# Kernel tuning notes

Hardware: AMD Instinct MI355X
Metric: run time of the kernel (lower is better)

The kernel has to match this reference:

```python
import jax, jax.numpy as jnp
import numpy as np

B, D_IN, UNITS = 4096, 1024, 1024


def setup_inputs() -> dict:
    key = jax.random.key(0)
    ks = jax.random.split(key, 8)
    scale = 1.0 / np.sqrt(D_IN + UNITS)
    return {
        "inputs": jax.random.normal(ks[0], (B, D_IN), jnp.float32),
        "hidden_state": jax.random.normal(ks[1], (B, UNITS), jnp.float32),
        "cell_state": jax.random.normal(ks[2], (B, UNITS), jnp.float32),
        "W_f": jax.random.normal(ks[3], (D_IN + UNITS, UNITS), jnp.float32) * scale,
        "b_f": jnp.ones((UNITS,), jnp.float32),  # forget gate bias initialized to ones
        "W_i": jax.random.normal(ks[4], (D_IN + UNITS, UNITS), jnp.float32) * scale,
        "b_i": jnp.zeros((UNITS,), jnp.float32),
        "W_c": jax.random.normal(ks[5], (D_IN + UNITS, UNITS), jnp.float32) * scale,
        "b_c": jnp.zeros((UNITS,), jnp.float32),
        "W_o": jax.random.normal(ks[6], (D_IN + UNITS, UNITS), jnp.float32) * scale,
        "b_o": jnp.zeros((UNITS,), jnp.float32),
    }


def reference(inputs, hidden_state, cell_state, W_f, b_f, W_i, b_i, W_c, b_c, W_o, b_o):
    # concat (hidden, inputs) along feature axis -> [B, UNITS + D_IN]
    x = jnp.concatenate((hidden_state, inputs), axis=1)
    # fuse the 4 gate projections into one GEMM: [B, 4*UNITS]
    W = jnp.concatenate((W_f, W_i, W_c, W_o), axis=1)
    b = jnp.concatenate((b_f, b_i, b_c, b_o), axis=0)
    gates = x @ W + b
    f, i, c, o = jnp.split(gates, 4, axis=1)
    forget_gate = jax.nn.sigmoid(f)
    input_gate = jax.nn.sigmoid(i)
    state_candidates = jnp.tanh(c)
    output_gate = jax.nn.sigmoid(o)
    new_cell = forget_gate * cell_state + input_gate * state_candidates
    new_hidden = output_gate * jnp.tanh(new_cell)
    return (new_hidden, new_cell)
```

## Files before the change

kernel.cpp:

```cpp
#include <hip/hip_runtime.h>

#define MDIM 4096
#define KDIM 2048
#define UDIM 1024
#define CMOFF (MDIM * UDIM)
#define NK 64
#define THREADS 512

typedef __bf16 bfrag __attribute__((ext_vector_type(8)));
typedef float f32x4 __attribute__((ext_vector_type(4)));

#define GLDS(gsrc, ldst)                                                                  \
  __builtin_amdgcn_global_load_lds((const __attribute__((address_space(1))) void*)(gsrc), \
                                   (__attribute__((address_space(3))) void*)(ldst), 16, 0, 0)

__device__ __forceinline__ unsigned short f2bf(float x) {
  unsigned int u = __float_as_uint(x);
  unsigned int r = (u + 0x7fffu + ((u >> 16) & 1u)) >> 16;
  return (unsigned short)r;
}

__device__ __forceinline__ float fast_sigmoid(float x) { return 1.f / (1.f + __expf(-x)); }

__device__ __forceinline__ float fast_tanh(float x) {
  float ax = fabsf(x);
  float e = __expf(-2.f * ax);
  float r = (1.f - e) / (1.f + e);
  return copysignf(r, x);
}

__global__ void pack_x(const float* __restrict__ hidden, const float* __restrict__ inputs,
                       unsigned short* __restrict__ A) {
  int t = blockIdx.x * blockDim.x + threadIdx.x;
  int e = t * 4;
  int m = e >> 11;
  int c = e & 2047;
  const float* src = (c < 1024) ? (hidden + m * 1024 + c) : (inputs + m * 1024 + (c - 1024));
  float4 v = *(const float4*)src;
  ushort4 o;
  o.x = f2bf(v.x);
  o.y = f2bf(v.y);
  o.z = f2bf(v.z);
  o.w = f2bf(v.w);
  *(ushort4*)(A + e) = o;
}

__global__ void pack_w(const float* __restrict__ Wf, const float* __restrict__ Wi,
                       const float* __restrict__ Wc, const float* __restrict__ Wo,
                       unsigned short* __restrict__ Wt) {
  __shared__ float tile[32][33];
  const int k0 = blockIdx.x * 32;
  const int u0 = blockIdx.y * 32;
  const int g = blockIdx.z;
  const float* W = (g == 0) ? Wf : (g == 1) ? Wi : (g == 2) ? Wc : Wo;
  const int t = threadIdx.x;
  {
    int kk = t >> 3, uu = (t & 7) * 4;
    float4 v = *(const float4*)(W + (k0 + kk) * UDIM + u0 + uu);
    tile[kk][uu + 0] = v.x;
    tile[kk][uu + 1] = v.y;
    tile[kk][uu + 2] = v.z;
    tile[kk][uu + 3] = v.w;
  }
  __syncthreads();
  {
    int ur = t >> 3, k4 = (t & 7) * 4;
    ushort4 o;
    o.x = f2bf(tile[k4 + 0][ur]);
    o.y = f2bf(tile[k4 + 1][ur]);
    o.z = f2bf(tile[k4 + 2][ur]);
    o.w = f2bf(tile[k4 + 3][ur]);
    *(ushort4*)(Wt + (size_t)(g * UDIM + u0 + ur) * KDIM + k0 + k4) = o;
  }
}

__global__ __launch_bounds__(THREADS, 2) void lstm_gemm(
    const unsigned short* __restrict__ A, const unsigned short* __restrict__ Wt,
    const float* __restrict__ bf_, const float* __restrict__ bi_,
    const float* __restrict__ bc_, const float* __restrict__ bo_,
    const float* __restrict__ cell, float* __restrict__ out) {
  extern __shared__ __bf16 lds[];

  const int tid = threadIdx.x;
  const int lane = tid & 63;
  const int wid = tid >> 6;
  const int wr = wid >> 2;
  const int wc = wid & 3;
  const int lrow = lane & 15;
  const int gb = lane >> 4;

  const int wg = blockIdx.x;
  const int swz = (wg & 7) * 32 + (wg >> 3);
  const int m0 = (swz >> 4) * 256;
  const int bn = swz & 15;

  const int G0 = tid, G1 = THREADS + tid;
  const int ar0 = G0 >> 2, ar1 = G1 >> 2;
  const unsigned short* aS0 =
      A + (size_t)(m0 + ar0) * KDIM + (((G0 & 3) ^ ((ar0 >> 1) & 3)) * 8);
  const unsigned short* aS1 =
      A + (size_t)(m0 + ar1) * KDIM + (((G1 & 3) ^ ((ar1 >> 1) & 3)) * 8);
  const int nr0 = G0 >> 2, nr1 = G1 >> 2;
  const int u_0 = bn * 64 + ((nr0 >> 6) << 4) + (nr0 & 15);
  const int u_1 = bn * 64 + ((nr1 >> 6) << 4) + (nr1 & 15);
  const int g_0 = (nr0 >> 4) & 3;
  const int g_1 = (nr1 >> 4) & 3;
  const unsigned short* bS0 =
      Wt + (size_t)(g_0 * UDIM + u_0) * KDIM + (((G0 & 3) ^ ((nr0 >> 1) & 3)) * 8);
  const unsigned short* bS1 =
      Wt + (size_t)(g_1 * UDIM + u_1) * KDIM + (((G1 & 3) ^ ((nr1 >> 1) & 3)) * 8);

  int aoff[8];
#pragma unroll
  for (int mi = 0; mi < 8; ++mi) {
    const int R = wr * 128 + mi * 16 + lrow;
    aoff[mi] = R * 32 + ((gb ^ ((R >> 1) & 3)) * 8);
  }
  int boff[4];
#pragma unroll
  for (int nf = 0; nf < 4; ++nf) {
    const int n = wc * 64 + nf * 16 + lrow;
    boff[nf] = 8192 + n * 32 + ((gb ^ ((n >> 1) & 3)) * 8);
  }

  f32x4 acc[8][4];
#pragma unroll
  for (int mi = 0; mi < 8; ++mi)
#pragma unroll
    for (int nf = 0; nf < 4; ++nf) acc[mi][nf] = (f32x4){0.f, 0.f, 0.f, 0.f};

#define STAGE_A(T)                                     \
  do {                                                 \
    __bf16* dst_ = lds + ((T) & 3) * 16384;            \
    GLDS(aS0 + (T) * 32, dst_ + G0 * 8);               \
    GLDS(aS1 + (T) * 32, dst_ + G1 * 8);               \
  } while (0)
#define STAGE_B(T)                                     \
  do {                                                 \
    __bf16* dst_ = lds + ((T) & 3) * 16384 + 8192;     \
    GLDS(bS0 + (T) * 32, dst_ + G0 * 8);               \
    GLDS(bS1 + (T) * 32, dst_ + G1 * 8);               \
  } while (0)

  STAGE_A(0);
  STAGE_B(0);
  STAGE_A(1);
  STAGE_B(1);
  STAGE_A(2);
  STAGE_B(2);
  __builtin_amdgcn_sched_barrier(0);
  asm volatile("s_waitcnt vmcnt(8)" ::: "memory");
  __builtin_amdgcn_s_barrier();
  __builtin_amdgcn_sched_barrier(0);

#define TILE_BODY(T, DO_STAGE, WAITCODE)                                                       \
  do {                                                                                         \
    __bf16* ldsr_ = lds + ((T) & 3) * 16384;                                                   \
    bfrag Af[8];                                                                               \
    _Pragma("unroll") for (int mi = 0; mi < 8; ++mi) Af[mi] = *(const bfrag*)(ldsr_ + aoff[mi]); \
    bfrag Bf0 = *(const bfrag*)(ldsr_ + boff[0]);                                              \
    bfrag Bf1 = *(const bfrag*)(ldsr_ + boff[1]);                                              \
    if (DO_STAGE) STAGE_A((T) + 3);                                                            \
    __builtin_amdgcn_sched_barrier(0);                                                         \
    __builtin_amdgcn_s_barrier();                                                              \
    __builtin_amdgcn_sched_barrier(0);                                                         \
    __builtin_amdgcn_s_setprio(1);                                                             \
    _Pragma("unroll") for (int mi = 0; mi < 8; ++mi) acc[mi][0] =                              \
        __builtin_amdgcn_mfma_f32_16x16x32_bf16(Af[mi], Bf0, acc[mi][0], 0, 0, 0);             \
    _Pragma("unroll") for (int mi = 0; mi < 8; ++mi) acc[mi][1] =                              \
        __builtin_amdgcn_mfma_f32_16x16x32_bf16(Af[mi], Bf1, acc[mi][1], 0, 0, 0);             \
    __builtin_amdgcn_s_setprio(0);                                                             \
    __builtin_amdgcn_sched_barrier(0);                                                         \
    __builtin_amdgcn_s_barrier();                                                              \
    __builtin_amdgcn_sched_barrier(0);                                                         \
    bfrag Bf2 = *(const bfrag*)(ldsr_ + boff[2]);                                              \
    bfrag Bf3 = *(const bfrag*)(ldsr_ + boff[3]);                                              \
    if (DO_STAGE) STAGE_B((T) + 3);                                                            \
    __builtin_amdgcn_sched_barrier(0);                                                         \
    __builtin_amdgcn_s_barrier();                                                              \
    __builtin_amdgcn_sched_barrier(0);                                                         \
    __builtin_amdgcn_s_setprio(1);                                                             \
    _Pragma("unroll") for (int mi = 0; mi < 8; ++mi) acc[mi][2] =                              \
        __builtin_amdgcn_mfma_f32_16x16x32_bf16(Af[mi], Bf2, acc[mi][2], 0, 0, 0);             \
    _Pragma("unroll") for (int mi = 0; mi < 8; ++mi) acc[mi][3] =                              \
        __builtin_amdgcn_mfma_f32_16x16x32_bf16(Af[mi], Bf3, acc[mi][3], 0, 0, 0);             \
    __builtin_amdgcn_s_setprio(0);                                                             \
    __builtin_amdgcn_sched_barrier(0);                                                         \
    WAITCODE;                                                                                  \
    __builtin_amdgcn_s_barrier();                                                              \
    __builtin_amdgcn_sched_barrier(0);                                                         \
  } while (0)

  for (int t = 0; t <= NK - 4; ++t) {
    TILE_BODY(t, 1, asm volatile("s_waitcnt vmcnt(8)" ::: "memory"));
  }
  TILE_BODY(NK - 3, 0, asm volatile("s_waitcnt vmcnt(4)" ::: "memory"));
  TILE_BODY(NK - 2, 0, asm volatile("s_waitcnt vmcnt(0)" ::: "memory"));
  TILE_BODY(NK - 1, 0, );

  const int u = bn * 64 + wc * 16 + lrow;
  const float fb = bf_[u], ib = bi_[u], cb = bc_[u], ob = bo_[u];
  const int rbase = m0 + wr * 128 + (lane >> 4) * 4;
#pragma unroll
  for (int mi = 0; mi < 8; ++mi) {
#pragma unroll
    for (int j = 0; j < 4; ++j) {
      const int m = rbase + mi * 16 + j;
      float pf = acc[mi][0][j] + fb;
      float pi = acc[mi][1][j] + ib;
      float pc = acc[mi][2][j] + cb;
      float po = acc[mi][3][j] + ob;
      float fg = fast_sigmoid(pf);
      float ig = fast_sigmoid(pi);
      float cc = fast_tanh(pc);
      float og = fast_sigmoid(po);
      float cold = cell[(size_t)m * UDIM + u];
      float cnew = fg * cold + ig * cc;
      out[(size_t)m * UDIM + u] = og * fast_tanh(cnew);
      out[CMOFF + (size_t)m * UDIM + u] = cnew;
    }
  }
}

extern "C" void kernel_launch(void* const* d_in, const int* in_sizes, int n_in,
                              void* d_out, int out_size, void* d_ws, size_t ws_size,
                              hipStream_t stream) {
  const float* inputs = (const float*)d_in[0];
  const float* hidden = (const float*)d_in[1];
  const float* cell = (const float*)d_in[2];
  const float* Wf = (const float*)d_in[3];
  const float* bf = (const float*)d_in[4];
  const float* Wi = (const float*)d_in[5];
  const float* bi = (const float*)d_in[6];
  const float* Wc = (const float*)d_in[7];
  const float* bc = (const float*)d_in[8];
  const float* Wo = (const float*)d_in[9];
  const float* bo = (const float*)d_in[10];
  float* out = (float*)d_out;

  unsigned short* Abf = (unsigned short*)d_ws;
  unsigned short* Wt = Abf + (size_t)MDIM * KDIM;

  pack_x<<<(MDIM * KDIM / 4) / 256, 256, 0, stream>>>(hidden, inputs, Abf);
  pack_w<<<dim3(KDIM / 32, UDIM / 32, 4), 256, 0, stream>>>(Wf, Wi, Wc, Wo, Wt);
  lstm_gemm<<<dim3(256), dim3(THREADS), 131072, stream>>>(Abf, Wt, bf, bi, bc, bo, cell, out);
}
```

Before: 92.34 us.

## Restructure GEMM main loop: split MFMA phases by M halves, unroll by four

The per-tile body now loads all four B fragments and half of the A fragments first, runs 16 MFMAs, then loads the other half of A and runs the remaining 16. Before, all eight A fragments were loaded up front and the work was split by N. The main loop is unrolled by four with compile-time LDS ring slots, which removes the runtime (T&3) address arithmetic, and the sched_barrier fences are dropped so the compiler can interleave freely. This should lower peak fragment register pressure and LDS-read latency before the first MFMA. The cost is that the compiler may reorder loads across the hand-placed barriers.

```diff
diff --git a/kernel.cpp b/kernel.cpp
--- a/kernel.cpp
+++ b/kernel.cpp
@@ -129,74 +129,71 @@
 #pragma unroll
     for (int nf = 0; nf < 4; ++nf) acc[mi][nf] = (f32x4){0.f, 0.f, 0.f, 0.f};
 
-#define STAGE_A(T)                                     \
-  do {                                                 \
-    __bf16* dst_ = lds + ((T) & 3) * 16384;            \
-    GLDS(aS0 + (T) * 32, dst_ + G0 * 8);               \
-    GLDS(aS1 + (T) * 32, dst_ + G1 * 8);               \
+#define STAGE_A(T, SR)                        \
+  do {                                        \
+    __bf16* dst_ = lds + (SR) * 16384;        \
+    GLDS(aS0 + (T) * 32, dst_ + G0 * 8);      \
+    GLDS(aS1 + (T) * 32, dst_ + G1 * 8);      \
   } while (0)
-#define STAGE_B(T)                                     \
-  do {                                                 \
-    __bf16* dst_ = lds + ((T) & 3) * 16384 + 8192;     \
-    GLDS(bS0 + (T) * 32, dst_ + G0 * 8);               \
-    GLDS(bS1 + (T) * 32, dst_ + G1 * 8);               \
+#define STAGE_B(T, SR)                        \
+  do {                                        \
+    __bf16* dst_ = lds + (SR) * 16384 + 8192; \
+    GLDS(bS0 + (T) * 32, dst_ + G0 * 8);      \
+    GLDS(bS1 + (T) * 32, dst_ + G1 * 8);      \
   } while (0)
 
-  STAGE_A(0);
-  STAGE_B(0);
-  STAGE_A(1);
-  STAGE_B(1);
-  STAGE_A(2);
-  STAGE_B(2);
-  __builtin_amdgcn_sched_barrier(0);
+  STAGE_A(0, 0);
+  STAGE_B(0, 0);
+  STAGE_A(1, 1);
+  STAGE_B(1, 1);
+  STAGE_A(2, 2);
+  STAGE_B(2, 2);
   asm volatile("s_waitcnt vmcnt(8)" ::: "memory");
   __builtin_amdgcn_s_barrier();
-  __builtin_amdgcn_sched_barrier(0);
-
-#define TILE_BODY(T, DO_STAGE, WAITCODE)                                                       \
-  do {                                                                                         \
-    __bf16* ldsr_ = lds + ((T) & 3) * 16384;                                                   \
-    bfrag Af[8];                                                                               \
-    _Pragma("unroll") for (int mi = 0; mi < 8; ++mi) Af[mi] = *(const bfrag*)(ldsr_ + aoff[mi]); \
-    bfrag Bf0 = *(const bfrag*)(ldsr_ + boff[0]);                                              \
-    bfrag Bf1 = *(const bfrag*)(ldsr_ + boff[1]);                                              \
-    if (DO_STAGE) STAGE_A((T) + 3);                                                            \
-    __builtin_amdgcn_sched_barrier(0);                                                         \
-    __builtin_amdgcn_s_barrier();                                                              \
-    __builtin_amdgcn_sched_barrier(0);                                                         \
-    __builtin_amdgcn_s_setprio(1);                                                             \
-    _Pragma("unroll") for (int mi = 0; mi < 8; ++mi) acc[mi][0] =                              \
-        __builtin_amdgcn_mfma_f32_16x16x32_bf16(Af[mi], Bf0, acc[mi][0], 0, 0, 0);             \
-    _Pragma("unroll") for (int mi = 0; mi < 8; ++mi) acc[mi][1] =                              \
-        __builtin_amdgcn_mfma_f32_16x16x32_bf16(Af[mi], Bf1, acc[mi][1], 0, 0, 0);             \
-    __builtin_amdgcn_s_setprio(0);                                                             \
-    __builtin_amdgcn_sched_barrier(0);                                                         \
-    __builtin_amdgcn_s_barrier();                                                              \
-    __builtin_amdgcn_sched_barrier(0);                                                         \
-    bfrag Bf2 = *(const bfrag*)(ldsr_ + boff[2]);                                              \
-    bfrag Bf3 = *(const bfrag*)(ldsr_ + boff[3]);                                              \
-    if (DO_STAGE) STAGE_B((T) + 3);                                                            \
-    __builtin_amdgcn_sched_barrier(0);                                                         \
-    __builtin_amdgcn_s_barrier();                                                              \
-    __builtin_amdgcn_sched_barrier(0);                                                         \
-    __builtin_amdgcn_s_setprio(1);                                                             \
-    _Pragma("unroll") for (int mi = 0; mi < 8; ++mi) acc[mi][2] =                              \
-        __builtin_amdgcn_mfma_f32_16x16x32_bf16(Af[mi], Bf2, acc[mi][2], 0, 0, 0);             \
-    _Pragma("unroll") for (int mi = 0; mi < 8; ++mi) acc[mi][3] =                              \
-        __builtin_amdgcn_mfma_f32_16x16x32_bf16(Af[mi], Bf3, acc[mi][3], 0, 0, 0);             \
-    __builtin_amdgcn_s_setprio(0);                                                             \
-    __builtin_amdgcn_sched_barrier(0);                                                         \
-    WAITCODE;                                                                                  \
-    __builtin_amdgcn_s_barrier();                                                              \
-    __builtin_amdgcn_sched_barrier(0);                                                         \
+
+#define TILE_BODY(T, R, SR, DO_STAGE, WAITCODE)                                        \
+  do {                                                                                 \
+    __bf16* ldsr_ = lds + (R) * 16384;                                                 \
+    bfrag Am[4], Bm[4];                                                                \
+    _Pragma("unroll") for (int mi = 0; mi < 4; ++mi) Am[mi] =                          \
+        *(const bfrag*)(ldsr_ + aoff[mi]);                                             \
+    _Pragma("unroll") for (int nf = 0; nf < 4; ++nf) Bm[nf] =                          \
+        *(const bfrag*)(ldsr_ + boff[nf]);                                             \
+    if (DO_STAGE) STAGE_A((T) + 3, SR);                                                \
+    __builtin_amdgcn_s_barrier();                                                      \
+    __builtin_amdgcn_s_setprio(1);                                                     \
+    _Pragma("unroll") for (int mi = 0; mi < 4; ++mi)                                   \
+        _Pragma("unroll") for (int nf = 0; nf < 4; ++nf) acc[mi][nf] =                 \
+            __builtin_amdgcn_mfma_f32_16x16x32_bf16(Am[mi], Bm[nf], acc[mi][nf], 0, 0, 0); \
+    __builtin_amdgcn_s_setprio(0);                                                     \
+    bfrag A2[4];                                                                       \
+    _Pragma("unroll") for (int mi = 0; mi < 4; ++mi) A2[mi] =                          \
+        *(const bfrag*)(ldsr_ + aoff[4 + mi]);                                         \
+    if (DO_STAGE) STAGE_B((T) + 3, SR);                                                \
+    __builtin_amdgcn_s_barrier();                                                      \
+    __builtin_amdgcn_s_setprio(1);                                                     \
+    _Pragma("unroll") for (int mi = 0; mi < 4; ++mi)                                   \
+        _Pragma("unroll") for (int nf = 0; nf < 4; ++nf) acc[4 + mi][nf] =             \
+            __builtin_amdgcn_mfma_f32_16x16x32_bf16(A2[mi], Bm[nf], acc[4 + mi][nf], 0, 0, 0); \
+    __builtin_amdgcn_s_setprio(0);                                                     \
+    WAITCODE;                                                                          \
+    __builtin_amdgcn_s_barrier();                                                      \
   } while (0)
 
-  for (int t = 0; t <= NK - 4; ++t) {
-    TILE_BODY(t, 1, asm volatile("s_waitcnt vmcnt(8)" ::: "memory"));
-  }
-  TILE_BODY(NK - 3, 0, asm volatile("s_waitcnt vmcnt(4)" ::: "memory"));
-  TILE_BODY(NK - 2, 0, asm volatile("s_waitcnt vmcnt(0)" ::: "memory"));
-  TILE_BODY(NK - 1, 0, );
+#define VM8 asm volatile("s_waitcnt vmcnt(8)" ::: "memory")
+#define VM4 asm volatile("s_waitcnt vmcnt(4)" ::: "memory")
+#define VM0 asm volatile("s_waitcnt vmcnt(0)" ::: "memory")
+
+  for (int t = 0; t < NK - 4; t += 4) {
+    TILE_BODY(t + 0, 0, 3, 1, VM8);
+    TILE_BODY(t + 1, 1, 0, 1, VM8);
+    TILE_BODY(t + 2, 2, 1, 1, VM8);
+    TILE_BODY(t + 3, 3, 2, 1, VM8);
+  }
+  TILE_BODY(NK - 4, 0, 3, 1, VM8);
+  TILE_BODY(NK - 3, 1, 0, 0, VM4);
+  TILE_BODY(NK - 2, 2, 0, 0, VM0);
+  TILE_BODY(NK - 1, 3, 0, 0, );
 
   const int u = bn * 64 + wc * 16 + lrow;
   const float fb = bf_[u], ib = bi_[u], cb = bc_[u], ob = bo_[u];
```

Measured after the change: 89.82 us. 1.03x faster.
